# Kernel optimization log

Measured on AMD Instinct MI355X. Metric: run time of the kernel, lower is better.

Reference implementation:

```python
import jax, jax.numpy as jnp
import numpy as np

STRIDE = (2, 2)  # from init_kwargs


def setup_inputs() -> dict:
    key = jax.random.key(0)
    kx, kw_, kb = jax.random.split(key, 3)
    x = jax.random.normal(kx, (8, 256, 64, 64), dtype=jnp.float32)
    weight = jax.random.normal(kw_, (128, 256, 4, 4), dtype=jnp.float32) * 0.02
    bias = jax.random.normal(kb, (128, 4, 4), dtype=jnp.float32) * 0.01
    return {"x": x, "weight": weight, "bias": bias}


def reference(x, weight, bias):
    # x: (b, i, h, w); weight: (o, i, kh, kw); bias: (o, kh, kw)
    b, c, h, w = x.shape
    o, _, kh, kw = weight.shape
    sh, sw = STRIDE
    # Outer-product contraction: (b, o, kh, kw, h, w)
    y = jnp.einsum('bihw,oixy->boxyhw', x, weight)
    # Bias is added per kernel position BEFORE the overlap-add fold,
    # so overlapping output pixels accumulate multiple bias copies
    # (faithful to the original module).
    y = y + bias[None, :, :, :, None, None]
    nh = (h - 1) * sh + kh
    nw = (w - 1) * sw + kw
    out = jnp.zeros((b, o, nh, nw), dtype=x.dtype)
    # fold: overlap-add scatter over the kh*kw kernel positions (small fixed loop)
    for ky in range(kh):
        for kxp in range(kw):
            out = out.at[:, :,
                         ky:ky + (h - 1) * sh + 1:sh,
                         kxp:kxp + (w - 1) * sw + 1:sw].add(y[:, :, ky, kxp])
    return out
```

## Files before the change

kernel.cpp:

```cpp
#include <hip/hip_runtime.h>
#include <stdint.h>
#include <stddef.h>

#define GLOBAL_AS __attribute__((address_space(1)))
#define LDS_AS    __attribute__((address_space(3)))

typedef __bf16 bf16x8 __attribute__((ext_vector_type(8)));
typedef float  f32x4  __attribute__((ext_vector_type(4)));

constexpr int NB = 8, CI = 256, H_ = 64, W_ = 64, CO = 128;
constexpr int OH = 130, OW = 130;
constexpr int PU = 65;
constexpr int PAD = 66;
constexpr int NPIX = PU * PU;
constexpr int NTILES = 34;

constexpr size_t XPAD_ELEMS = (size_t)NB * PAD * PAD * CI;
constexpr size_t XPAD_BYTES = XPAD_ELEMS * 2;
constexpr size_t WT_OFF     = XPAD_BYTES;

__device__ __forceinline__ void gload_lds16(const void* g, void* l) {
  __builtin_amdgcn_global_load_lds((GLOBAL_AS void*)g, (LDS_AS void*)l, 16, 0, 0);
}

__global__ void prep_x(const float* __restrict__ x, __bf16* __restrict__ xp) {
  __shared__ float tile[64][65];
  const int h   = blockIdx.x;
  const int bat = blockIdx.y;
  const int t   = threadIdx.x;
  for (int ch = 0; ch < 4; ++ch) {
    const int i0 = ch * 64;
    const float* src = x + (((size_t)(bat * CI + i0)) * H_ + h) * W_;
    if (ch) __syncthreads();
#pragma unroll
    for (int r = 0; r < 4; ++r) {
      int ii = r * 16 + (t >> 4);
      int ww = (t & 15) * 4;
      float4 v = *(const float4*)(src + (size_t)ii * H_ * W_ + ww);
      tile[ii][ww] = v.x; tile[ii][ww + 1] = v.y; tile[ii][ww + 2] = v.z; tile[ii][ww + 3] = v.w;
    }
    __syncthreads();
    __bf16* dst = xp + ((size_t)(bat * PAD + h + 1) * PAD + 1) * CI + i0;
#pragma unroll
    for (int r = 0; r < 2; ++r) {
      int s  = r * 256 + t;
      int ww = s >> 3;
      int ig = (s & 7) * 8;
      bf16x8 o;
#pragma unroll
      for (int k = 0; k < 8; ++k) o[k] = (__bf16)tile[ig + k][ww];
      *(bf16x8*)(dst + (size_t)ww * CI + ig) = o;
    }
  }
}

__global__ void prep_w2(const float* __restrict__ w, __bf16* __restrict__ wt2) {
  int tid = blockIdx.x * 256 + threadIdx.x;
  int i   = tid & 255;
  int tap = (tid >> 8) & 3;
  int row = (tid >> 10) & 255;
  int py  = tid >> 18;
  int a = tap >> 1, c = tap & 1;
  int o = row >> 1, px = row & 1;
  wt2[tid] = (__bf16)w[(size_t)(o * CI + i) * 16 + (py + 2 * a) * 4 + (px + 2 * c)];
}

__global__ __launch_bounds__(512) void deconv_mfma(
    const __bf16* __restrict__ xp, const __bf16* __restrict__ wt2,
    const float* __restrict__ bias, float* __restrict__ out) {
  const int wg    = blockIdx.x;
  const int nt_i  = wg % NTILES;
  const int bat   = (wg / NTILES) % 8;
  const int py    = wg / (NTILES * 8);
  const int nBase = nt_i * 128;

  __shared__ alignas(16) __bf16 lds[2][12288];

  const int t    = threadIdx.x;
  const int wid  = t >> 6, lane = t & 63;
  const int lr   = lane & 15, kg = lane >> 4;
  const int wr   = wid >> 1, wc = wid & 1;

  const int mA   = t >> 2;
  const int kstA = (t & 3) ^ ((mA >> 1) & 3);
  const __bf16* srcA = wt2 + ((size_t)py * 256 + mA) * 1024 + kstA * 8;

  int pix = nBase + mA;
  if (pix > NPIX - 1) pix = NPIX - 1;
  const int uB = pix / PU, vB = pix % PU;
  const __bf16* srcB = xp + ((size_t)(bat * PAD + uB + 1) * PAD + (vB + 1)) * CI + kstA * 8;

  const int swz = (lr >> 1) & 3;
  int offA[4], offB[4];
#pragma unroll
  for (int mt = 0; mt < 4; ++mt)
    offA[mt] = (wr * 64 + mt * 16 + lr) * 32 + ((kg ^ swz) * 8);
#pragma unroll
  for (int nt = 0; nt < 4; ++nt)
    offB[nt] = 8192 + (wc * 64 + nt * 16 + lr) * 32 + ((kg ^ swz) * 8);

  f32x4 acc[4][4] = {};

  auto stage = [&](int buf, int s) {
    const int ic = (s & 7) * 32;
    const int a  = s >> 4, c = (s >> 3) & 1;
    const __bf16* sa = srcA + s * 32;
    const __bf16* sb = srcB + ic - (size_t)(a * PAD + c) * CI;
    __bf16* l = &lds[buf][0];
    gload_lds16(sa,                    l + (size_t)t * 8);
    gload_lds16(sa + 128 * 1024,       l + (size_t)t * 8 + 4096);
    gload_lds16(sb,                    l + 8192 + (size_t)t * 8);
  };

  stage(0, 0);
  __syncthreads();
  int cur = 0;
  for (int s = 0; s < 32; ++s) {
    if (s < 31) stage(cur ^ 1, s + 1);
    const __bf16* base = &lds[cur][0];
    bf16x8 af[4], bf[4];
#pragma unroll
    for (int mt = 0; mt < 4; ++mt) af[mt] = *(const bf16x8*)(base + offA[mt]);
#pragma unroll
    for (int nt = 0; nt < 4; ++nt) bf[nt] = *(const bf16x8*)(base + offB[nt]);
#pragma unroll
    for (int mt = 0; mt < 4; ++mt)
#pragma unroll
      for (int nt = 0; nt < 4; ++nt)
        acc[mt][nt] = __builtin_amdgcn_mfma_f32_16x16x32_bf16(af[mt], bf[nt], acc[mt][nt], 0, 0, 0);
    __syncthreads();
    cur ^= 1;
  }

#pragma unroll
  for (int mt = 0; mt < 4; ++mt) {
    const int rbase = wr * 64 + mt * 16 + kg * 4;
    const int o0 = rbase >> 1, o1 = o0 + 1;
#pragma unroll
    for (int nt = 0; nt < 4; ++nt) {
      const int n = nBase + wc * 64 + nt * 16 + lr;
      if (n < NPIX) {
        const int u = n / PU, v = n % PU;
        const int oy = 2 * u + py;
        const bool a0 = (u <= 63), a1 = (u >= 1);
        const bool c0 = (v <= 63), c1 = (v >= 1);
        auto bs = [&](int o, int px) {
          const float* bp = bias + (size_t)o * 16;
          float s0 = 0.f;
          if (a0 && c0) s0 += bp[py * 4 + px];
          if (a0 && c1) s0 += bp[py * 4 + px + 2];
          if (a1 && c0) s0 += bp[(py + 2) * 4 + px];
          if (a1 && c1) s0 += bp[(py + 2) * 4 + px + 2];
          return s0;
        };
        const size_t b0 = ((size_t)(bat * CO + o0) * OH + oy) * OW + 2 * v;
        const size_t b1 = ((size_t)(bat * CO + o1) * OH + oy) * OW + 2 * v;
        float2 w0, w1;
        w0.x = acc[mt][nt][0] + bs(o0, 0);
        w0.y = acc[mt][nt][1] + bs(o0, 1);
        w1.x = acc[mt][nt][2] + bs(o1, 0);
        w1.y = acc[mt][nt][3] + bs(o1, 1);
        *(float2*)(out + b0) = w0;
        *(float2*)(out + b1) = w1;
      }
    }
  }
}

extern "C" void kernel_launch(void* const* d_in, const int* in_sizes, int n_in,
                              void* d_out, int out_size, void* d_ws, size_t ws_size,
                              hipStream_t stream) {
  const float* x    = (const float*)d_in[0];
  const float* w    = (const float*)d_in[1];
  const float* bias = (const float*)d_in[2];
  float* out = (float*)d_out;
  char* ws = (char*)d_ws;
  __bf16* xpad = (__bf16*)ws;
  __bf16* wt2  = (__bf16*)(ws + WT_OFF);

  hipMemsetAsync(xpad, 0, XPAD_BYTES, stream);
  prep_x<<<dim3(64, 8), 256, 0, stream>>>(x, xpad);
  prep_w2<<<dim3(2048), 256, 0, stream>>>(w, wt2);
  deconv_mfma<<<dim3(544), 512, 0, stream>>>(xpad, wt2, bias, out);
}
```

Baseline: 188.7 us.

## Enlarge GEMM tiles, flatten batch into N, deepen pipeline, fuse pad zeroing

```diff
diff --git a/kernel.cpp b/kernel.cpp
--- a/kernel.cpp
+++ b/kernel.cpp
@@ -13,7 +13,8 @@
 constexpr int PU = 65;
 constexpr int PAD = 66;
 constexpr int NPIX = PU * PU;
-constexpr int NTILES = 34;
+constexpr int NTOT = NB * NPIX;
+constexpr int NT_N = 133;
 
 constexpr size_t XPAD_ELEMS = (size_t)NB * PAD * PAD * CI;
 constexpr size_t XPAD_BYTES = XPAD_ELEMS * 2;
@@ -28,6 +29,20 @@
   const int h   = blockIdx.x;
   const int bat = blockIdx.y;
   const int t   = threadIdx.x;
+  if (h >= 64) {
+    const int row = (h == 64) ? 0 : 65;
+    __bf16* dst = xp + (size_t)(bat * PAD + row) * PAD * CI;
+    bf16x8 z = {};
+    for (int idx = t; idx < PAD * CI / 8; idx += 256)
+      *(bf16x8*)(dst + (size_t)idx * 8) = z;
+    return;
+  }
+  if (t < 64) {
+    __bf16* rowp = xp + (size_t)(bat * PAD + h + 1) * PAD * CI;
+    bf16x8 z = {};
+    int half = t >> 5, part = t & 31;
+    *(bf16x8*)(rowp + (size_t)half * 65 * CI + part * 8) = z;
+  }
   for (int ch = 0; ch < 4; ++ch) {
     const int i0 = ch * 64;
     const float* src = x + (((size_t)(bat * CI + i0)) * H_ + h) * W_;
@@ -65,82 +80,99 @@
   wt2[tid] = (__bf16)w[(size_t)(o * CI + i) * 16 + (py + 2 * a) * 4 + (px + 2 * c)];
 }
 
-__global__ __launch_bounds__(512) void deconv_mfma(
+__global__ __launch_bounds__(512, 2) void deconv_mfma(
     const __bf16* __restrict__ xp, const __bf16* __restrict__ wt2,
     const float* __restrict__ bias, float* __restrict__ out) {
-  const int wg    = blockIdx.x;
-  const int nt_i  = wg % NTILES;
-  const int bat   = (wg / NTILES) % 8;
-  const int py    = wg / (NTILES * 8);
-  const int nBase = nt_i * 128;
-
-  __shared__ alignas(16) __bf16 lds[2][12288];
+  const int wg   = blockIdx.x;
+  const int py   = wg / NT_N;
+  const int nt_i = wg % NT_N;
+  const int nBase = nt_i * 256;
+
+  __shared__ alignas(16) __bf16 lds[2][32768];
 
   const int t    = threadIdx.x;
   const int wid  = t >> 6, lane = t & 63;
   const int lr   = lane & 15, kg = lane >> 4;
-  const int wr   = wid >> 1, wc = wid & 1;
-
-  const int mA   = t >> 2;
-  const int kstA = (t & 3) ^ ((mA >> 1) & 3);
-  const __bf16* srcA = wt2 + ((size_t)py * 256 + mA) * 1024 + kstA * 8;
-
-  int pix = nBase + mA;
-  if (pix > NPIX - 1) pix = NPIX - 1;
-  const int uB = pix / PU, vB = pix % PU;
-  const __bf16* srcB = xp + ((size_t)(bat * PAD + uB + 1) * PAD + (vB + 1)) * CI + kstA * 8;
-
-  const int swz = (lr >> 1) & 3;
-  int offA[4], offB[4];
-#pragma unroll
-  for (int mt = 0; mt < 4; ++mt)
-    offA[mt] = (wr * 64 + mt * 16 + lr) * 32 + ((kg ^ swz) * 8);
-#pragma unroll
-  for (int nt = 0; nt < 4; ++nt)
-    offB[nt] = 8192 + (wc * 64 + nt * 16 + lr) * 32 + ((kg ^ swz) * 8);
-
-  f32x4 acc[4][4] = {};
+  const int wm   = wid >> 1, wn = wid & 1;
+
+  const int rowT = t >> 3;
+  const int grp  = (t & 7) ^ ((t >> 3) & 7);
+  const __bf16* srcA = wt2 + ((size_t)(py * 256 + rowT)) * 1024 + grp * 8;
+  const __bf16* srcB[4];
+#pragma unroll
+  for (int cc = 0; cc < 4; ++cc) {
+    int n = nBase + rowT + cc * 64;
+    if (n > NTOT - 1) n = NTOT - 1;
+    const int bat = n / NPIX, pr = n % NPIX;
+    const int u = pr / PU, v = pr % PU;
+    srcB[cc] = xp + ((size_t)(bat * PAD + u + 1) * PAD + (v + 1)) * CI + grp * 8;
+  }
+
+  int offA[2][4], offB[2][8];
+#pragma unroll
+  for (int ksub = 0; ksub < 2; ++ksub) {
+    const int gx = ((ksub * 4 + kg) ^ (lr & 7)) * 16;
+#pragma unroll
+    for (int mt = 0; mt < 4; ++mt)
+      offA[ksub][mt] = (wm * 64 + mt * 16 + lr) * 128 + gx;
+#pragma unroll
+    for (int nt = 0; nt < 8; ++nt)
+      offB[ksub][nt] = 32768 + (wn * 128 + nt * 16 + lr) * 128 + gx;
+  }
+
+  f32x4 acc[4][8] = {};
 
   auto stage = [&](int buf, int s) {
-    const int ic = (s & 7) * 32;
-    const int a  = s >> 4, c = (s >> 3) & 1;
-    const __bf16* sa = srcA + s * 32;
-    const __bf16* sb = srcB + ic - (size_t)(a * PAD + c) * CI;
-    __bf16* l = &lds[buf][0];
-    gload_lds16(sa,                    l + (size_t)t * 8);
-    gload_lds16(sa + 128 * 1024,       l + (size_t)t * 8 + 4096);
-    gload_lds16(sb,                    l + 8192 + (size_t)t * 8);
+    char* l = (char*)&lds[buf][0];
+    const size_t koff = (size_t)s * 64;
+#pragma unroll
+    for (int cc = 0; cc < 4; ++cc)
+      gload_lds16(srcA + (size_t)cc * 65536 + koff, l + (t + cc * 512) * 16);
+    const int tap = s >> 2;
+    const int shift = ((tap >> 1) * PAD + (tap & 1)) * CI;
+    const int ik = (s & 3) * 64;
+#pragma unroll
+    for (int cc = 0; cc < 4; ++cc)
+      gload_lds16(srcB[cc] + ik - shift, l + 32768 + (t + cc * 512) * 16);
   };
 
   stage(0, 0);
-  __syncthreads();
-  int cur = 0;
-  for (int s = 0; s < 32; ++s) {
-    if (s < 31) stage(cur ^ 1, s + 1);
-    const __bf16* base = &lds[cur][0];
-    bf16x8 af[4], bf[4];
-#pragma unroll
-    for (int mt = 0; mt < 4; ++mt) af[mt] = *(const bf16x8*)(base + offA[mt]);
-#pragma unroll
-    for (int nt = 0; nt < 4; ++nt) bf[nt] = *(const bf16x8*)(base + offB[nt]);
-#pragma unroll
-    for (int mt = 0; mt < 4; ++mt)
-#pragma unroll
-      for (int nt = 0; nt < 4; ++nt)
-        acc[mt][nt] = __builtin_amdgcn_mfma_f32_16x16x32_bf16(af[mt], bf[nt], acc[mt][nt], 0, 0, 0);
-    __syncthreads();
-    cur ^= 1;
+  stage(1, 1);
+  for (int s = 0; s < 16; ++s) {
+    const int cur = s & 1;
+    if (s < 15) asm volatile("s_waitcnt vmcnt(8)" ::: "memory");
+    else        asm volatile("s_waitcnt vmcnt(0)" ::: "memory");
+    asm volatile("s_barrier" ::: "memory");
+    const char* base = (const char*)&lds[cur][0];
+#pragma unroll
+    for (int ksub = 0; ksub < 2; ++ksub) {
+      bf16x8 af[4], bfr[8];
+#pragma unroll
+      for (int mt = 0; mt < 4; ++mt) af[mt]  = *(const bf16x8*)(base + offA[ksub][mt]);
+#pragma unroll
+      for (int nt = 0; nt < 8; ++nt) bfr[nt] = *(const bf16x8*)(base + offB[ksub][nt]);
+      __builtin_amdgcn_s_setprio(1);
+#pragma unroll
+      for (int mt = 0; mt < 4; ++mt)
+#pragma unroll
+        for (int nt = 0; nt < 8; ++nt)
+          acc[mt][nt] = __builtin_amdgcn_mfma_f32_16x16x32_bf16(af[mt], bfr[nt], acc[mt][nt], 0, 0, 0);
+      __builtin_amdgcn_s_setprio(0);
+    }
+    asm volatile("s_barrier" ::: "memory");
+    if (s < 14) stage(cur, s + 2);
   }
 
 #pragma unroll
   for (int mt = 0; mt < 4; ++mt) {
-    const int rbase = wr * 64 + mt * 16 + kg * 4;
+    const int rbase = wm * 64 + mt * 16 + kg * 4;
     const int o0 = rbase >> 1, o1 = o0 + 1;
 #pragma unroll
-    for (int nt = 0; nt < 4; ++nt) {
-      const int n = nBase + wc * 64 + nt * 16 + lr;
-      if (n < NPIX) {
-        const int u = n / PU, v = n % PU;
+    for (int nt = 0; nt < 8; ++nt) {
+      const int n = nBase + wn * 128 + nt * 16 + lr;
+      if (n < NTOT) {
+        const int bat = n / NPIX, pr = n % NPIX;
+        const int u = pr / PU, v = pr % PU;
         const int oy = 2 * u + py;
         const bool a0 = (u <= 63), a1 = (u >= 1);
         const bool c0 = (v <= 63), c1 = (v >= 1);
@@ -178,8 +210,7 @@
   __bf16* xpad = (__bf16*)ws;
   __bf16* wt2  = (__bf16*)(ws + WT_OFF);
 
-  hipMemsetAsync(xpad, 0, XPAD_BYTES, stream);
-  prep_x<<<dim3(64, 8), 256, 0, stream>>>(x, xpad);
+  prep_x<<<dim3(66, 8), 256, 0, stream>>>(x, xpad);
   prep_w2<<<dim3(2048), 256, 0, stream>>>(w, wt2);
-  deconv_mfma<<<dim3(544), 512, 0, stream>>>(xpad, wt2, bias, out);
-}
+  deconv_mfma<<<dim3(2 * NT_N), 512, 0, stream>>>(xpad, wt2, bias, out);
+}
```

Measured after the change: 226.1 us. 19.8% more time.

## Materialize im2col B matrix and flatten GEMM over batch with 128x128 tiles

Applied to the files above, without the earlier changes.

```diff
diff --git a/kernel.cpp b/kernel.cpp
--- a/kernel.cpp
+++ b/kernel.cpp
@@ -13,11 +13,13 @@
 constexpr int PU = 65;
 constexpr int PAD = 66;
 constexpr int NPIX = PU * PU;
-constexpr int NTILES = 34;
-
-constexpr size_t XPAD_ELEMS = (size_t)NB * PAD * PAD * CI;
-constexpr size_t XPAD_BYTES = XPAD_ELEMS * 2;
-constexpr size_t WT_OFF     = XPAD_BYTES;
+constexpr int NTOT = NB * NPIX;
+constexpr int NT_N = 265;
+
+constexpr size_t XPAD_BYTES = (size_t)NB * PAD * PAD * CI * 2;
+constexpr size_t A_OFF      = XPAD_BYTES;
+constexpr size_t A_BYTES    = (size_t)512 * 1024 * 2;
+constexpr size_t B_OFF      = A_OFF + A_BYTES;
 
 __device__ __forceinline__ void gload_lds16(const void* g, void* l) {
   __builtin_amdgcn_global_load_lds((GLOBAL_AS void*)g, (LDS_AS void*)l, 16, 0, 0);
@@ -28,6 +30,20 @@
   const int h   = blockIdx.x;
   const int bat = blockIdx.y;
   const int t   = threadIdx.x;
+  if (h >= 64) {
+    const int row = (h == 64) ? 0 : 65;
+    __bf16* dst = xp + (size_t)(bat * PAD + row) * PAD * CI;
+    bf16x8 z = {};
+    for (int idx = t; idx < PAD * CI / 8; idx += 256)
+      *(bf16x8*)(dst + (size_t)idx * 8) = z;
+    return;
+  }
+  if (t < 64) {
+    __bf16* rowp = xp + (size_t)(bat * PAD + h + 1) * PAD * CI;
+    bf16x8 z = {};
+    int half = t >> 5, part = t & 31;
+    *(bf16x8*)(rowp + (size_t)half * 65 * CI + part * 8) = z;
+  }
   for (int ch = 0; ch < 4; ++ch) {
     const int i0 = ch * 64;
     const float* src = x + (((size_t)(bat * CI + i0)) * H_ + h) * W_;
@@ -54,41 +70,53 @@
   }
 }
 
-__global__ void prep_w2(const float* __restrict__ w, __bf16* __restrict__ wt2) {
-  int tid = blockIdx.x * 256 + threadIdx.x;
-  int i   = tid & 255;
-  int tap = (tid >> 8) & 3;
-  int row = (tid >> 10) & 255;
-  int py  = tid >> 18;
-  int a = tap >> 1, c = tap & 1;
-  int o = row >> 1, px = row & 1;
-  wt2[tid] = (__bf16)w[(size_t)(o * CI + i) * 16 + (py + 2 * a) * 4 + (px + 2 * c)];
-}
-
-__global__ __launch_bounds__(512) void deconv_mfma(
-    const __bf16* __restrict__ xp, const __bf16* __restrict__ wt2,
+__global__ void build_ab(const float* __restrict__ w, const __bf16* __restrict__ xp,
+                         __bf16* __restrict__ amat, __bf16* __restrict__ bmat) {
+  const int bid = blockIdx.x;
+  const int t   = threadIdx.x;
+  if (bid < 16900) {
+    const int g = bid * 256 + t;
+    const int n = g >> 7, c = g & 127;
+    const int tap = c >> 5, ic = c & 31;
+    const int a = tap >> 1, cc = tap & 1;
+    const int bat = n / NPIX, pr = n % NPIX;
+    const int u = pr / PU, v = pr % PU;
+    const __bf16* src = xp + (((size_t)(bat * PAD + u + 1 - a)) * PAD + (v + 1 - cc)) * CI + ic * 8;
+    *(bf16x8*)(bmat + (size_t)n * 1024 + (size_t)c * 8) = *(const bf16x8*)src;
+  } else {
+    const int tid = (bid - 16900) * 256 + t;
+    const int i   = tid & 255;
+    const int tap = (tid >> 8) & 3;
+    const int row = (tid >> 10) & 255;
+    const int py  = tid >> 18;
+    const int a = tap >> 1, c = tap & 1;
+    const int o = row >> 1, px = row & 1;
+    amat[tid] = (__bf16)w[(size_t)(o * CI + i) * 16 + (py + 2 * a) * 4 + (px + 2 * c)];
+  }
+}
+
+__global__ __launch_bounds__(256) void deconv_mfma(
+    const __bf16* __restrict__ amat, const __bf16* __restrict__ bmat,
     const float* __restrict__ bias, float* __restrict__ out) {
-  const int wg    = blockIdx.x;
-  const int nt_i  = wg % NTILES;
-  const int bat   = (wg / NTILES) % 8;
-  const int py    = wg / (NTILES * 8);
+  const int wg   = blockIdx.x;
+  const int mt_i = wg & 3;
+  const int nt_i = wg >> 2;
   const int nBase = nt_i * 128;
 
-  __shared__ alignas(16) __bf16 lds[2][12288];
+  __shared__ alignas(16) __bf16 lds[2][8192];
 
   const int t    = threadIdx.x;
   const int wid  = t >> 6, lane = t & 63;
   const int lr   = lane & 15, kg = lane >> 4;
   const int wr   = wid >> 1, wc = wid & 1;
 
-  const int mA   = t >> 2;
-  const int kstA = (t & 3) ^ ((mA >> 1) & 3);
-  const __bf16* srcA = wt2 + ((size_t)py * 256 + mA) * 1024 + kstA * 8;
-
-  int pix = nBase + mA;
-  if (pix > NPIX - 1) pix = NPIX - 1;
-  const int uB = pix / PU, vB = pix % PU;
-  const __bf16* srcB = xp + ((size_t)(bat * PAD + uB + 1) * PAD + (vB + 1)) * CI + kstA * 8;
+  const int m0   = t >> 2;
+  const int kst  = (t & 3) ^ ((m0 >> 1) & 3);
+  const __bf16* srcA  = amat + ((size_t)(mt_i * 128 + m0)) * 1024 + kst * 8;
+  int nA = nBase + m0;       if (nA > NTOT - 1) nA = NTOT - 1;
+  int nB2 = nBase + m0 + 64; if (nB2 > NTOT - 1) nB2 = NTOT - 1;
+  const __bf16* srcB  = bmat + (size_t)nA  * 1024 + kst * 8;
+  const __bf16* srcB2 = bmat + (size_t)nB2 * 1024 + kst * 8;
 
   const int swz = (lr >> 1) & 3;
   int offA[4], offB[4];
@@ -97,19 +125,17 @@
     offA[mt] = (wr * 64 + mt * 16 + lr) * 32 + ((kg ^ swz) * 8);
 #pragma unroll
   for (int nt = 0; nt < 4; ++nt)
-    offB[nt] = 8192 + (wc * 64 + nt * 16 + lr) * 32 + ((kg ^ swz) * 8);
+    offB[nt] = 4096 + (wc * 64 + nt * 16 + lr) * 32 + ((kg ^ swz) * 8);
 
   f32x4 acc[4][4] = {};
 
   auto stage = [&](int buf, int s) {
-    const int ic = (s & 7) * 32;
-    const int a  = s >> 4, c = (s >> 3) & 1;
-    const __bf16* sa = srcA + s * 32;
-    const __bf16* sb = srcB + ic - (size_t)(a * PAD + c) * CI;
+    const size_t ko = (size_t)s * 32;
     __bf16* l = &lds[buf][0];
-    gload_lds16(sa,                    l + (size_t)t * 8);
-    gload_lds16(sa + 128 * 1024,       l + (size_t)t * 8 + 4096);
-    gload_lds16(sb,                    l + 8192 + (size_t)t * 8);
+    gload_lds16(srcA  + ko,              l + (size_t)t * 8);
+    gload_lds16(srcA  + 64 * 1024 + ko,  l + (size_t)t * 8 + 2048);
+    gload_lds16(srcB  + ko,              l + 4096 + (size_t)t * 8);
+    gload_lds16(srcB2 + ko,              l + 4096 + (size_t)t * 8 + 2048);
   };
 
   stage(0, 0);
@@ -118,29 +144,31 @@
   for (int s = 0; s < 32; ++s) {
     if (s < 31) stage(cur ^ 1, s + 1);
     const __bf16* base = &lds[cur][0];
-    bf16x8 af[4], bf[4];
-#pragma unroll
-    for (int mt = 0; mt < 4; ++mt) af[mt] = *(const bf16x8*)(base + offA[mt]);
-#pragma unroll
-    for (int nt = 0; nt < 4; ++nt) bf[nt] = *(const bf16x8*)(base + offB[nt]);
+    bf16x8 af[4], bfr[4];
+#pragma unroll
+    for (int mt = 0; mt < 4; ++mt) af[mt]  = *(const bf16x8*)(base + offA[mt]);
+#pragma unroll
+    for (int nt = 0; nt < 4; ++nt) bfr[nt] = *(const bf16x8*)(base + offB[nt]);
 #pragma unroll
     for (int mt = 0; mt < 4; ++mt)
 #pragma unroll
       for (int nt = 0; nt < 4; ++nt)
-        acc[mt][nt] = __builtin_amdgcn_mfma_f32_16x16x32_bf16(af[mt], bf[nt], acc[mt][nt], 0, 0, 0);
+        acc[mt][nt] = __builtin_amdgcn_mfma_f32_16x16x32_bf16(af[mt], bfr[nt], acc[mt][nt], 0, 0, 0);
     __syncthreads();
     cur ^= 1;
   }
 
+  const int py = mt_i >> 1;
 #pragma unroll
   for (int mt = 0; mt < 4; ++mt) {
-    const int rbase = wr * 64 + mt * 16 + kg * 4;
+    const int rbase = (mt_i & 1) * 128 + wr * 64 + mt * 16 + kg * 4;
     const int o0 = rbase >> 1, o1 = o0 + 1;
 #pragma unroll
     for (int nt = 0; nt < 4; ++nt) {
       const int n = nBase + wc * 64 + nt * 16 + lr;
-      if (n < NPIX) {
-        const int u = n / PU, v = n % PU;
+      if (n < NTOT) {
+        const int bat = n / NPIX, pr = n % NPIX;
+        const int u = pr / PU, v = pr % PU;
         const int oy = 2 * u + py;
         const bool a0 = (u <= 63), a1 = (u >= 1);
         const bool c0 = (v <= 63), c1 = (v >= 1);
@@ -176,10 +204,10 @@
   float* out = (float*)d_out;
   char* ws = (char*)d_ws;
   __bf16* xpad = (__bf16*)ws;
-  __bf16* wt2  = (__bf16*)(ws + WT_OFF);
-
-  hipMemsetAsync(xpad, 0, XPAD_BYTES, stream);
-  prep_x<<<dim3(64, 8), 256, 0, stream>>>(x, xpad);
-  prep_w2<<<dim3(2048), 256, 0, stream>>>(w, wt2);
-  deconv_mfma<<<dim3(544), 512, 0, stream>>>(xpad, wt2, bias, out);
-}
+  __bf16* amat = (__bf16*)(ws + A_OFF);
+  __bf16* bmat = (__bf16*)(ws + B_OFF);
+
+  prep_x<<<dim3(66, 8), 256, 0, stream>>>(x, xpad);
+  build_ab<<<dim3(16900 + 2048), 256, 0, stream>>>(w, xpad, amat, bmat);
+  deconv_mfma<<<dim3(4 * NT_N), 256, 0, stream>>>(amat, bmat, bias, out);
+}
```

Result: slower. 203.4 us (+7.8%).
